# Performance work log

Measured on AMD Instinct MI355X. Metric: run time of the kernel, lower is better.

The kernel has to match this reference:

```python
import jax, jax.numpy as jnp
import numpy as np

# ---- config (mirrors CoInHead init + TARGET_ASSIGNER_CONFIG) ----
PCR0, PCR1 = -51.2, -51.2          # point_cloud_range x/y min
VX, VY = 0.05, 0.05                # voxel_size x/y
STRIDE = 4                         # FEATURE_MAP_STRIDE
FW, FH = 512, 512                  # feature_map_size [x, y] = grid/stride
NUM_CLASSES = 10
NUM_MAX_OBJS = 500
OVERLAP = 0.1                      # GAUSSIAN_OVERLAP
MIN_RADIUS = 2
RMAX = 16                          # static cap on radius (covers all synthetic boxes)
K = 2 * RMAX + 1                   # fixed gaussian patch size
EPS = float(np.finfo(np.float32).eps)
BATCH = 16


def _gaussian_radius(height, width, min_overlap):
    # faithful to centernet_utils.gaussian_radius (OpenPCDet)
    b1 = height + width
    c1 = width * height * (1.0 - min_overlap) / (1.0 + min_overlap)
    sq1 = jnp.sqrt(jnp.maximum(b1 * b1 - 4.0 * c1, 0.0))
    r1 = (b1 + sq1) / 2.0

    b2 = 2.0 * (height + width)
    c2 = (1.0 - min_overlap) * width * height
    sq2 = jnp.sqrt(jnp.maximum(b2 * b2 - 16.0 * c2, 0.0))
    r2 = (b2 + sq2) / 2.0

    a3 = 4.0 * min_overlap
    b3 = -2.0 * min_overlap * (height + width)
    c3 = (min_overlap - 1.0) * width * height
    sq3 = jnp.sqrt(jnp.maximum(b3 * b3 - 4.0 * a3 * c3, 0.0))
    r3 = (b3 + sq3) / (2.0 * a3)
    return jnp.minimum(jnp.minimum(r1, r2), r3)


def setup_inputs() -> dict:
    key = jax.random.key(0)
    ks = jax.random.split(key, 8)
    B, M = BATCH, NUM_MAX_OBJS
    x = jax.random.uniform(ks[0], (B, M), minval=-50.0, maxval=50.0)
    y = jax.random.uniform(ks[1], (B, M), minval=-50.0, maxval=50.0)
    z = jax.random.uniform(ks[2], (B, M), minval=-2.0, maxval=1.0)
    dx = jax.random.uniform(ks[3], (B, M), minval=0.5, maxval=6.0)
    dy = jax.random.uniform(ks[4], (B, M), minval=0.5, maxval=6.0)
    dz = jax.random.uniform(ks[5], (B, M), minval=0.5, maxval=3.0)
    heading = jax.random.uniform(ks[6], (B, M), minval=-np.pi, maxval=np.pi)
    cls = jax.random.randint(ks[7], (B, M), 1, NUM_CLASSES + 1).astype(jnp.float32)
    gt_boxes = jnp.stack([x, y, z, dx, dy, dz, heading, cls], axis=-1).astype(jnp.float32)
    return {"gt_boxes": gt_boxes}


def reference(gt_boxes):
    # vectorized assign_target_of_single_head over (batch, objects)
    B, M, _ = gt_boxes.shape
    f32 = jnp.float32
    x, y, z = gt_boxes[..., 0], gt_boxes[..., 1], gt_boxes[..., 2]
    dx, dy, dz = gt_boxes[..., 3], gt_boxes[..., 4], gt_boxes[..., 5]
    heading = gt_boxes[..., 6]
    cls = (gt_boxes[..., 7] - 1.0).astype(jnp.int32)          # 0-based class id

    coord_x = jnp.clip((x - PCR0) / VX / STRIDE, 0.0, FW - 0.5)
    coord_y = jnp.clip((y - PCR1) / VY / STRIDE, 0.0, FH - 0.5)
    cxi = coord_x.astype(jnp.int32)
    cyi = coord_y.astype(jnp.int32)

    dxf = dx / VX / STRIDE
    dyf = dy / VY / STRIDE
    radius = _gaussian_radius(dxf, dyf, OVERLAP)
    radius = jnp.clip(radius.astype(jnp.int32), MIN_RADIUS, RMAX)  # (B, M)

    valid = (dxf > 0) & (dyf > 0) & (cxi >= 0) & (cxi <= FW) & (cyi >= 0) & (cyi <= FH)

    # fixed KxK gaussian patch centered on the integer center
    off = jnp.arange(K, dtype=jnp.int32) - RMAX
    oi = off[:, None]                                   # (K,1) row offset
    oj = off[None, :]                                   # (1,K) col offset
    sigma = (2.0 * radius.astype(f32) + 1.0) / 6.0      # diameter/6
    d2 = (oi * oi + oj * oj).astype(f32)                # (K,K)
    g = jnp.exp(-d2[None, None] / (2.0 * sigma[..., None, None] ** 2))  # (B,M,K,K)
    g = jnp.where(g < EPS, 0.0, g)                      # gaussian_2d eps truncation

    r_bm = radius[..., None, None]
    within = (jnp.abs(oi)[None, None] <= r_bm) & (jnp.abs(oj)[None, None] <= r_bm)
    yy = cyi[..., None, None] + oi[None, None]          # (B,M,K,K)
    xx = cxi[..., None, None] + oj[None, None]
    inb = (yy >= 0) & (yy < FH) & (xx >= 0) & (xx < FW)
    vals = jnp.where(valid[..., None, None] & within & inb, g, 0.0)

    b_idx = jnp.arange(B, dtype=jnp.int32)[:, None, None, None]
    c_idx = jnp.clip(cls, 0, NUM_CLASSES - 1)[..., None, None]
    heatmap = jnp.zeros((B, NUM_CLASSES, FH, FW), f32).at[
        b_idx, c_idx, jnp.clip(yy, 0, FH - 1), jnp.clip(xx, 0, FW - 1)
    ].max(vals)

    inds = jnp.where(valid, cyi * FW + cxi, 0).astype(jnp.int64)
    mask = valid.astype(jnp.int64)

    vf = valid.astype(f32)[..., None]
    ret_boxes = jnp.stack([
        coord_x - cxi.astype(f32),
        coord_y - cyi.astype(f32),
        z,
        jnp.log(jnp.maximum(dx, 1e-12)),
        jnp.log(jnp.maximum(dy, 1e-12)),
        jnp.log(jnp.maximum(dz, 1e-12)),
        jnp.cos(heading),
        jnp.sin(heading),
    ], axis=-1) * vf                                     # (B,M,8)

    return heatmap, ret_boxes, inds, mask
```

## Files before the change

kernel.cpp:

```cpp
#include <hip/hip_runtime.h>
#include <hip/hip_bf16.h>

#define PCR0   (-51.2f)
#define PCR1   (-51.2f)
#define VX_    (0.05f)
#define VY_    (0.05f)
#define STRIDE_ 4.0f
#define FW_    512
#define FH_    512
#define NCLS   10
#define NOBJ   500
#define OVERLAP_ 0.1f
#define MINRAD 2
#define RMAX_  16
#define BATCH_ 16
#define EPS_   1.1920928955078125e-07f

#define HEATMAP_ELEMS  (BATCH_ * NCLS * FH_ * FW_)
#define RETBOX_OFF     HEATMAP_ELEMS
#define RETBOX_ELEMS   (BATCH_ * NOBJ * 8)
#define INDS_OFF       (RETBOX_OFF + RETBOX_ELEMS)
#define INDS_ELEMS     (BATCH_ * NOBJ)
#define MASK_OFF       (INDS_OFF + INDS_ELEMS)

__global__ void zero_heatmap(float4* __restrict__ hm4, int n4) {
    int idx = blockIdx.x * blockDim.x + threadIdx.x;
    int stride = gridDim.x * blockDim.x;
    float4 z = make_float4(0.f, 0.f, 0.f, 0.f);
    for (int i = idx; i < n4; i += stride) hm4[i] = z;
}

__global__ __launch_bounds__(256) void paint_objects(
        const float* __restrict__ gt,
        float* __restrict__ out)
{
    const int obj = blockIdx.x;
    const int b   = obj / NOBJ;

    const float* g8 = gt + (size_t)obj * 8;
    const float x  = g8[0], y  = g8[1], z  = g8[2];
    const float dx = g8[3], dy = g8[4], dz = g8[5];
    const float hd = g8[6], clsf = g8[7];

    float coord_x = fminf(fmaxf((x - PCR0) / VX_ / STRIDE_, 0.f), (float)FW_ - 0.5f);
    float coord_y = fminf(fmaxf((y - PCR1) / VY_ / STRIDE_, 0.f), (float)FH_ - 0.5f);
    int cxi = (int)coord_x;
    int cyi = (int)coord_y;

    float dxf = dx / VX_ / STRIDE_;
    float dyf = dy / VY_ / STRIDE_;

    const float h = dxf, w = dyf, o = OVERLAP_;
    float b1 = h + w;
    float c1 = w * h * (1.f - o) / (1.f + o);
    float r1 = (b1 + sqrtf(fmaxf(b1 * b1 - 4.f * c1, 0.f))) * 0.5f;
    float b2 = 2.f * (h + w);
    float c2 = (1.f - o) * w * h;
    float r2 = (b2 + sqrtf(fmaxf(b2 * b2 - 16.f * c2, 0.f))) * 0.5f;
    float a3 = 4.f * o;
    float b3 = -2.f * o * (h + w);
    float c3 = (o - 1.f) * w * h;
    float r3 = (b3 + sqrtf(fmaxf(b3 * b3 - 4.f * a3 * c3, 0.f))) / (2.f * a3);
    float radf = fminf(fminf(r1, r2), r3);
    int radius = (int)radf;
    radius = min(max(radius, MINRAD), RMAX_);

    bool valid = (dxf > 0.f) && (dyf > 0.f) &&
                 (cxi >= 0) && (cxi <= FW_) && (cyi >= 0) && (cyi <= FH_);

    if (threadIdx.x == 0) {
        float vf = valid ? 1.f : 0.f;
        float* rb = out + RETBOX_OFF + (size_t)obj * 8;
        rb[0] = (coord_x - (float)cxi) * vf;
        rb[1] = (coord_y - (float)cyi) * vf;
        rb[2] = z * vf;
        rb[3] = logf(fmaxf(dx, 1e-12f)) * vf;
        rb[4] = logf(fmaxf(dy, 1e-12f)) * vf;
        rb[5] = logf(fmaxf(dz, 1e-12f)) * vf;
        rb[6] = cosf(hd) * vf;
        rb[7] = sinf(hd) * vf;
        out[INDS_OFF + obj] = valid ? (float)(cyi * FW_ + cxi) : 0.f;
        out[MASK_OFF + obj] = vf;
    }

    if (!valid) return;

    float sigma = (2.f * (float)radius + 1.f) / 6.f;
    float denom = 2.f * sigma * sigma;
    int side = 2 * radius + 1;
    int npos = side * side;

    int cls_i = (int)(clsf - 1.0f);
    int c = min(max(cls_i, 0), NCLS - 1);
    float* hm = out + ((size_t)b * NCLS + c) * (size_t)(FH_ * FW_);

    for (int idx = threadIdx.x; idx < npos; idx += blockDim.x) {
        int i = idx / side - radius;
        int j = idx % side - radius;
        float d2 = (float)(i * i + j * j);
        float gv = expf(-d2 / denom);
        if (gv < EPS_) continue;
        int yy = cyi + i;
        int xx = cxi + j;
        if (yy < 0 || yy >= FH_ || xx < 0 || xx >= FW_) continue;
        atomicMax((int*)(hm + (size_t)yy * FW_ + xx), __float_as_int(gv));
    }
}

extern "C" void kernel_launch(void* const* d_in, const int* in_sizes, int n_in,
                              void* d_out, int out_size, void* d_ws, size_t ws_size,
                              hipStream_t stream) {
    const float* gt = (const float*)d_in[0];
    float* out = (float*)d_out;

    int n4 = HEATMAP_ELEMS / 4;
    zero_heatmap<<<4096, 256, 0, stream>>>((float4*)out, n4);

    paint_objects<<<BATCH_ * NOBJ, 256, 0, stream>>>(gt, out);
}
```

Before: 191.5 us.

## Bin objects into screen tiles and paint heatmap per tile without atomics

Replaces the zero-fill plus per-object atomicMax painting with a two-phase scheme. A first kernel computes per-object parameters and ret_boxes, then appends each object to per-batch 32x32 tile bins. A second kernel has each block own one tile, keep per-class maxima in registers and write every heatmap pixel once, which removes the separate zeroing pass and the global atomics. It needs a large workspace and falls back to the old path if the workspace is too small. Any bin holding more than 512 objects is silently truncated, and the ten-class register accumulator adds register pressure.

```diff
diff --git a/kernel.cpp b/kernel.cpp
--- a/kernel.cpp
+++ b/kernel.cpp
@@ -20,32 +20,38 @@
 #define RETBOX_OFF     HEATMAP_ELEMS
 #define RETBOX_ELEMS   (BATCH_ * NOBJ * 8)
 #define INDS_OFF       (RETBOX_OFF + RETBOX_ELEMS)
-#define INDS_ELEMS     (BATCH_ * NOBJ)
-#define MASK_OFF       (INDS_OFF + INDS_ELEMS)
-
-__global__ void zero_heatmap(float4* __restrict__ hm4, int n4) {
-    int idx = blockIdx.x * blockDim.x + threadIdx.x;
-    int stride = gridDim.x * blockDim.x;
-    float4 z = make_float4(0.f, 0.f, 0.f, 0.f);
-    for (int i = idx; i < n4; i += stride) hm4[i] = z;
-}
-
-__global__ __launch_bounds__(256) void paint_objects(
-        const float* __restrict__ gt,
-        float* __restrict__ out)
-{
-    const int obj = blockIdx.x;
-    const int b   = obj / NOBJ;
-
-    const float* g8 = gt + (size_t)obj * 8;
-    const float x  = g8[0], y  = g8[1], z  = g8[2];
-    const float dx = g8[3], dy = g8[4], dz = g8[5];
-    const float hd = g8[6], clsf = g8[7];
-
-    float coord_x = fminf(fmaxf((x - PCR0) / VX_ / STRIDE_, 0.f), (float)FW_ - 0.5f);
-    float coord_y = fminf(fmaxf((y - PCR1) / VY_ / STRIDE_, 0.f), (float)FH_ - 0.5f);
-    int cxi = (int)coord_x;
-    int cyi = (int)coord_y;
+#define MASK_OFF       (INDS_OFF + BATCH_ * NOBJ)
+
+#define TILE_  32
+#define TPB_   (FW_ / TILE_)
+#define NTILES (TPB_ * TPB_)
+#define CAP_   512
+
+#define CNT_BYTES   (BATCH_ * NTILES * 4)
+#define REC_OFF     CNT_BYTES
+#define REC_BYTES   (BATCH_ * NOBJ * 32)
+#define LIST_OFF    (REC_OFF + REC_BYTES)
+#define LIST_BYTES  ((size_t)BATCH_ * NTILES * CAP_ * 4)
+#define WS_NEEDED   (LIST_OFF + LIST_BYTES)
+
+struct __align__(16) ObjRec {
+    int   cxi, cyi, rad, cls;
+    float negInv;
+    int   valid;
+    float pad0, pad1;
+};
+
+__device__ __forceinline__ void obj_params(const float* g8,
+        float& coord_x, float& coord_y, int& cxi, int& cyi,
+        int& radius, bool& valid)
+{
+    const float x = g8[0], y = g8[1];
+    const float dx = g8[3], dy = g8[4];
+
+    coord_x = fminf(fmaxf((x - PCR0) / VX_ / STRIDE_, 0.f), (float)FW_ - 0.5f);
+    coord_y = fminf(fmaxf((y - PCR1) / VY_ / STRIDE_, 0.f), (float)FH_ - 0.5f);
+    cxi = (int)coord_x;
+    cyi = (int)coord_y;
 
     float dxf = dx / VX_ / STRIDE_;
     float dyf = dy / VY_ / STRIDE_;
@@ -62,11 +68,149 @@
     float c3 = (o - 1.f) * w * h;
     float r3 = (b3 + sqrtf(fmaxf(b3 * b3 - 4.f * a3 * c3, 0.f))) / (2.f * a3);
     float radf = fminf(fminf(r1, r2), r3);
-    int radius = (int)radf;
+    radius = (int)radf;
     radius = min(max(radius, MINRAD), RMAX_);
 
-    bool valid = (dxf > 0.f) && (dyf > 0.f) &&
-                 (cxi >= 0) && (cxi <= FW_) && (cyi >= 0) && (cyi <= FH_);
+    valid = (dxf > 0.f) && (dyf > 0.f) &&
+            (cxi >= 0) && (cxi <= FW_) && (cyi >= 0) && (cyi <= FH_);
+}
+
+__global__ void phaseA(const float* __restrict__ gt, float* __restrict__ out,
+                       int* __restrict__ cnt, int* __restrict__ lists,
+                       ObjRec* __restrict__ recs)
+{
+    int obj = blockIdx.x * blockDim.x + threadIdx.x;
+    if (obj >= BATCH_ * NOBJ) return;
+    int b = obj / NOBJ;
+
+    const float* g8 = gt + (size_t)obj * 8;
+    float coord_x, coord_y; int cxi, cyi, radius; bool valid;
+    obj_params(g8, coord_x, coord_y, cxi, cyi, radius, valid);
+
+    const float z = g8[2], dx = g8[3], dy = g8[4], dz = g8[5];
+    const float hd = g8[6], clsf = g8[7];
+
+    float vf = valid ? 1.f : 0.f;
+    float* rb = out + RETBOX_OFF + (size_t)obj * 8;
+    rb[0] = (coord_x - (float)cxi) * vf;
+    rb[1] = (coord_y - (float)cyi) * vf;
+    rb[2] = z * vf;
+    rb[3] = logf(fmaxf(dx, 1e-12f)) * vf;
+    rb[4] = logf(fmaxf(dy, 1e-12f)) * vf;
+    rb[5] = logf(fmaxf(dz, 1e-12f)) * vf;
+    rb[6] = cosf(hd) * vf;
+    rb[7] = sinf(hd) * vf;
+    out[INDS_OFF + obj] = valid ? (float)(cyi * FW_ + cxi) : 0.f;
+    out[MASK_OFF + obj] = vf;
+
+    int c = min(max((int)(clsf - 1.0f), 0), NCLS - 1);
+    float sigma = (2.f * (float)radius + 1.f) / 6.f;
+    float denom = 2.f * sigma * sigma;
+
+    ObjRec r;
+    r.cxi = cxi; r.cyi = cyi; r.rad = radius; r.cls = c;
+    r.negInv = -1.0f / denom;
+    r.valid = valid ? 1 : 0;
+    r.pad0 = 0.f; r.pad1 = 0.f;
+    recs[obj] = r;
+
+    if (!valid) return;
+
+    int tx0 = max(cxi - radius, 0) >> 5;
+    int tx1 = min(cxi + radius, FW_ - 1) >> 5;
+    int ty0 = max(cyi - radius, 0) >> 5;
+    int ty1 = min(cyi + radius, FH_ - 1) >> 5;
+    for (int ty = ty0; ty <= ty1; ++ty) {
+        for (int tx = tx0; tx <= tx1; ++tx) {
+            int bin = b * NTILES + ty * TPB_ + tx;
+            int pos = atomicAdd(&cnt[bin], 1);
+            if (pos < CAP_) lists[(size_t)bin * CAP_ + pos] = obj;
+        }
+    }
+}
+
+__global__ __launch_bounds__(256) void phaseB(
+        float* __restrict__ out,
+        const int* __restrict__ cnt, const int* __restrict__ lists,
+        const ObjRec* __restrict__ recs)
+{
+    int bid  = blockIdx.x;
+    int b    = bid >> 8;
+    int tile = bid & (NTILES - 1);
+    int ty = tile >> 4, tx = tile & (TPB_ - 1);
+
+    int lr  = threadIdx.x >> 3;
+    int lc  = (threadIdx.x & 7) << 2;
+    int py  = (ty << 5) + lr;
+    int px0 = (tx << 5) + lc;
+
+    float acc[NCLS][4];
+    #pragma unroll
+    for (int c = 0; c < NCLS; ++c) {
+        acc[c][0] = 0.f; acc[c][1] = 0.f; acc[c][2] = 0.f; acc[c][3] = 0.f;
+    }
+
+    int bin = b * NTILES + tile;
+    int n = cnt[bin]; if (n > CAP_) n = CAP_;
+    const int* lst = lists + (size_t)bin * CAP_;
+
+    for (int k2 = 0; k2 < n; ++k2) {
+        int o = lst[k2];
+        ObjRec r = recs[o];
+        int rad = r.rad;
+        int ry = py - r.cyi;
+        bool rowin = (ry >= -rad) && (ry <= rad);
+        float fy = (float)(ry * ry);
+
+        float val[4];
+        #pragma unroll
+        for (int k = 0; k < 4; ++k) {
+            int rx = px0 + k - r.cxi;
+            bool in = rowin && (rx >= -rad) && (rx <= rad);
+            float d2 = fy + (float)(rx * rx);
+            float g = expf(d2 * r.negInv);
+            val[k] = (in && g >= EPS_) ? g : 0.f;
+        }
+
+        int cu = __builtin_amdgcn_readfirstlane(r.cls);
+        #pragma unroll
+        for (int c = 0; c < NCLS; ++c) {
+            if (c == cu) {
+                #pragma unroll
+                for (int k = 0; k < 4; ++k)
+                    acc[c][k] = fmaxf(acc[c][k], val[k]);
+            }
+        }
+    }
+
+    size_t plane = (size_t)FH_ * FW_;
+    size_t base  = (size_t)b * NCLS * plane + (size_t)py * FW_ + px0;
+    #pragma unroll
+    for (int c = 0; c < NCLS; ++c) {
+        float4 v = make_float4(acc[c][0], acc[c][1], acc[c][2], acc[c][3]);
+        *(float4*)(out + base + (size_t)c * plane) = v;
+    }
+}
+
+__global__ void zero_heatmap(float4* __restrict__ hm4, int n4) {
+    int idx = blockIdx.x * blockDim.x + threadIdx.x;
+    int stride = gridDim.x * blockDim.x;
+    float4 z = make_float4(0.f, 0.f, 0.f, 0.f);
+    for (int i = idx; i < n4; i += stride) hm4[i] = z;
+}
+
+__global__ __launch_bounds__(256) void paint_objects(
+        const float* __restrict__ gt, float* __restrict__ out)
+{
+    const int obj = blockIdx.x;
+    const int b   = obj / NOBJ;
+    const float* g8 = gt + (size_t)obj * 8;
+
+    float coord_x, coord_y; int cxi, cyi, radius; bool valid;
+    obj_params(g8, coord_x, coord_y, cxi, cyi, radius, valid);
+
+    const float z = g8[2], dx = g8[3], dy = g8[4], dz = g8[5];
+    const float hd = g8[6], clsf = g8[7];
 
     if (threadIdx.x == 0) {
         float vf = valid ? 1.f : 0.f;
@@ -82,16 +226,13 @@
         out[INDS_OFF + obj] = valid ? (float)(cyi * FW_ + cxi) : 0.f;
         out[MASK_OFF + obj] = vf;
     }
-
     if (!valid) return;
 
     float sigma = (2.f * (float)radius + 1.f) / 6.f;
     float denom = 2.f * sigma * sigma;
     int side = 2 * radius + 1;
     int npos = side * side;
-
-    int cls_i = (int)(clsf - 1.0f);
-    int c = min(max(cls_i, 0), NCLS - 1);
+    int c = min(max((int)(clsf - 1.0f), 0), NCLS - 1);
     float* hm = out + ((size_t)b * NCLS + c) * (size_t)(FH_ * FW_);
 
     for (int idx = threadIdx.x; idx < npos; idx += blockDim.x) {
@@ -113,8 +254,18 @@
     const float* gt = (const float*)d_in[0];
     float* out = (float*)d_out;
 
-    int n4 = HEATMAP_ELEMS / 4;
-    zero_heatmap<<<4096, 256, 0, stream>>>((float4*)out, n4);
-
-    paint_objects<<<BATCH_ * NOBJ, 256, 0, stream>>>(gt, out);
-}
+    if (ws_size >= WS_NEEDED) {
+        int* cnt      = (int*)d_ws;
+        ObjRec* recs  = (ObjRec*)((char*)d_ws + REC_OFF);
+        int* lists    = (int*)((char*)d_ws + LIST_OFF);
+
+        hipMemsetAsync(cnt, 0, CNT_BYTES, stream);
+
+        phaseA<<<(BATCH_ * NOBJ + 255) / 256, 256, 0, stream>>>(gt, out, cnt, lists, recs);
+        phaseB<<<BATCH_ * NTILES, 256, 0, stream>>>(out, cnt, lists, recs);
+    } else {
+        int n4 = HEATMAP_ELEMS / 4;
+        zero_heatmap<<<4096, 256, 0, stream>>>((float4*)out, n4);
+        paint_objects<<<BATCH_ * NOBJ, 256, 0, stream>>>(gt, out);
+    }
+}
```

Measured after the change: 173.8 us. 9.2% less time.
